# Optimization experiments

Hardware: AMD Instinct MI355X
Metric: run time of the kernel (lower is better)

The kernel has to match this reference:

```python
import jax, jax.numpy as jnp
import numpy as np

NUM_HEADS = 8


def setup_inputs() -> dict:
    key = jax.random.key(0)
    ks = jax.random.split(key, 5)
    B, C, H, W = 2, 256, 64, 64
    # 0.02 scaling keeps logits in a sane range so softmax is not one-hot
    return {
        "x": jax.random.normal(ks[0], (B, C, H, W), dtype=jnp.float32),
        "w_qkv": jax.random.normal(ks[1], (3 * C, C), dtype=jnp.float32) * 0.02,
        "b_qkv": jax.random.normal(ks[2], (3 * C,), dtype=jnp.float32) * 0.02,
        "w_proj": jax.random.normal(ks[3], (C, C), dtype=jnp.float32) * 0.02,
        "b_proj": jax.random.normal(ks[4], (C,), dtype=jnp.float32) * 0.02,
    }


def reference(x, w_qkv, b_qkv, w_proj, b_proj):
    B, C, H, W = x.shape
    N = H * W
    h = NUM_HEADS
    d = C // h
    # 1x1 conv == per-pixel linear: (B,C,H,W) -> (B,3C,H,W)
    qkv = jnp.einsum('oc,bchw->bohw', w_qkv, x) + b_qkv[None, :, None, None]
    qkv = qkv.reshape(B, 3, h, d, N)
    # q,k,v: (B, h, N, d)
    q = jnp.swapaxes(qkv[:, 0], -2, -1)
    k = jnp.swapaxes(qkv[:, 1], -2, -1)
    v = jnp.swapaxes(qkv[:, 2], -2, -1)
    scale = d ** (-0.5)
    attn = jax.nn.softmax(jnp.einsum('bhnd,bhmd->bhnm', q, k) * scale, axis=-1)
    out = jnp.einsum('bhnm,bhmd->bhnd', attn, v)  # (B, h, N, d)
    # faithful to torch: transpose(1,2) -> (B,N,h,d), then row-major reshape to (B,C,H,W)
    out = jnp.swapaxes(out, 1, 2).reshape(B, C, H, W)
    out = jnp.einsum('oc,bchw->bohw', w_proj, out) + b_proj[None, :, None, None]
    return out
```

## Files before the change

### kernel.cpp

```cpp
#include <hip/hip_runtime.h>
#include <hip/hip_bf16.h>


typedef __bf16 bf16;
typedef __bf16 bf16x4 __attribute__((ext_vector_type(4)));
typedef __bf16 bf16x8 __attribute__((ext_vector_type(8)));
typedef float  f32x4  __attribute__((ext_vector_type(4)));
typedef short  s16x4  __attribute__((ext_vector_type(4)));

#if __has_builtin(__builtin_amdgcn_mfma_f32_16x16x16bf16_1k)
#define HAVE_MFMA16 1
#endif

#if __has_builtin(__builtin_amdgcn_exp2f)
#define EXP2(x) __builtin_amdgcn_exp2f(x)
#else
#define EXP2(x) exp2f(x)
#endif

#define NS 4096
#define QSCALE (0.17677669529663687f * 1.4426950408889634f)

static __device__ inline unsigned pack2(float a, float b) {
  union { bf16 h[2]; unsigned u; } v;
  v.h[0] = (bf16)a; v.h[1] = (bf16)b;
  return v.u;
}

__global__ __launch_bounds__(256) void qkv_fused(
    const float* __restrict__ x, const float* __restrict__ w,
    const float* __restrict__ bias,
    bf16* __restrict__ qbuf, bf16* __restrict__ kbuf, bf16* __restrict__ vbuf)
{
  __shared__ bf16 As[64 * 264];
  __shared__ bf16 Bs[64 * 264];
  const int n0 = blockIdx.x * 64, o0 = blockIdx.y * 64, b = blockIdx.z;
  const int t = threadIdx.x;
  const int wv = t >> 6, L = t & 63, quad = L >> 4, lb = L & 15;

  {
    unsigned* A32 = (unsigned*)As;
    const int nj = (t & 15) * 4;
#pragma unroll
    for (int p = 0; p < 8; p++) {
      const int c = p * 32 + (t >> 4) * 2;
      const float* xr = x + ((size_t)(b * 256 + c)) * NS + n0 + nj;
      f32x4 va = *(const f32x4*)xr;
      f32x4 vb = *(const f32x4*)(xr + NS);
#pragma unroll
      for (int i = 0; i < 4; i++)
        A32[(nj + i) * 132 + (c >> 1)] = pack2(va[i], vb[i]);
    }
  }
  {
    const int cj = (t & 15) * 16;
#pragma unroll
    for (int p = 0; p < 4; p++) {
      const int r = p * 16 + (t >> 4);
      const float* wr = w + (size_t)(o0 + r) * 256 + cj;
      f32x4 w0 = *(const f32x4*)wr,       w1 = *(const f32x4*)(wr + 4);
      f32x4 w2 = *(const f32x4*)(wr + 8), w3 = *(const f32x4*)(wr + 12);
      bf16x8 lo, hi;
#pragma unroll
      for (int i = 0; i < 4; i++) {
        lo[i] = (bf16)w0[i]; lo[4 + i] = (bf16)w1[i];
        hi[i] = (bf16)w2[i]; hi[4 + i] = (bf16)w3[i];
      }
      *(bf16x8*)&Bs[r * 264 + cj] = lo;
      *(bf16x8*)&Bs[r * 264 + cj + 8] = hi;
    }
  }
  __syncthreads();

  f32x4 acc[4] = {};
#pragma unroll
  for (int ks = 0; ks < 8; ks++) {
    const bf16x8 bfr = *(const bf16x8*)&Bs[(wv * 16 + lb) * 264 + ks * 32 + quad * 8];
#pragma unroll
    for (int a = 0; a < 4; a++) {
      const bf16x8 afr = *(const bf16x8*)&As[(a * 16 + lb) * 264 + ks * 32 + quad * 8];
      acc[a] = __builtin_amdgcn_mfma_f32_16x16x32_bf16(afr, bfr, acc[a], 0, 0, 0);
    }
  }

  const int comp = o0 >> 8;
  const int o = o0 + wv * 16 + lb;
  const float bv = bias[o];
  if (comp < 2) {
    bf16* dst = (comp == 0) ? qbuf : kbuf;
    const float sc = (comp == 0) ? QSCALE : 1.0f;
    const int hh = (o & 255) >> 5, dd = o & 31;
    const size_t base = ((size_t)b * 8 + hh) * NS;
#pragma unroll
    for (int a = 0; a < 4; a++)
#pragma unroll
      for (int r = 0; r < 4; r++) {
        const int n = n0 + a * 16 + quad * 4 + r;
        dst[(base + n) * 32 + dd] = (bf16)((acc[a][r] + bv) * sc);
      }
  } else {
    __syncthreads();
    bf16* Vt2 = As;
#pragma unroll
    for (int a = 0; a < 4; a++)
#pragma unroll
      for (int r = 0; r < 4; r++)
        Vt2[(wv * 16 + lb) * 72 + a * 16 + quad * 4 + r] = (bf16)(acc[a][r] + bv);
    __syncthreads();
    const int row = t & 63;
    const int o2 = o0 + row;
    const int hh2 = (o2 & 255) >> 5, dd2 = o2 & 31;
    const int hc = (t >> 6) * 16;
    bf16x8 v0 = *(const bf16x8*)&Vt2[row * 72 + hc];
    bf16x8 v1 = *(const bf16x8*)&Vt2[row * 72 + hc + 8];
    bf16* vd = vbuf + (((size_t)b * 8 + hh2) * 32 + dd2) * NS + n0 + hc;
    *(bf16x8*)vd = v0;
    *(bf16x8*)(vd + 8) = v1;
  }
}

#define VT_OFF 2560
#define KV_SZ  (2560 + 32 * 72)

__global__ __launch_bounds__(256) void attn_kernel(
    const bf16* __restrict__ qbuf, const bf16* __restrict__ kbuf,
    const bf16* __restrict__ vbuf, float* __restrict__ pbuf,
    float* __restrict__ lbuf)
{
  __shared__ bf16 KV[2][KV_SZ];
#ifndef HAVE_MFMA16
  __shared__ bf16 Ps[4][16 * 72];
#endif

  const int qb = blockIdx.x;
  const int bh = blockIdx.y;
  const int half = blockIdx.z;
  const int kv0 = half * 2048;
  const bf16* Q  = qbuf + (size_t)bh * NS * 32;
  const bf16* K  = kbuf + (size_t)bh * NS * 32 + (size_t)kv0 * 32;
  const bf16* Vt = vbuf + (size_t)bh * 32 * NS + kv0;

  const int t = threadIdx.x;
  const int wv = t >> 6, L = t & 63, quad = L >> 4, lb = L & 15;
  const int qrow = qb * 128 + wv * 32;

  const bf16x8 qfrag0 = *(const bf16x8*)(Q + (size_t)(qrow + lb) * 32 + quad * 8);
  const bf16x8 qfrag1 = *(const bf16x8*)(Q + (size_t)(qrow + 16 + lb) * 32 + quad * 8);

  const int koff = (t >> 2) * 40 + (t & 3) * 8;
  const int voff = VT_OFF + (t >> 3) * 72 + (t & 7) * 8;
  const bf16* gk = K + (size_t)(t >> 2) * 32 + (t & 3) * 8;
  const bf16* gv = Vt + (size_t)(t >> 3) * NS + (t & 7) * 8;

  bf16x8 regk = *(const bf16x8*)gk;
  bf16x8 regv = *(const bf16x8*)gv;

  f32x4 oa0 = {0.f, 0.f, 0.f, 0.f}, oa1 = {0.f, 0.f, 0.f, 0.f};
  f32x4 oa2 = {0.f, 0.f, 0.f, 0.f}, oa3 = {0.f, 0.f, 0.f, 0.f};
  f32x4 oa4 = {0.f, 0.f, 0.f, 0.f}, oa5 = {0.f, 0.f, 0.f, 0.f};
  const f32x4 zero4 = {0.f, 0.f, 0.f, 0.f};
#ifdef HAVE_MFMA16
  const s16x4 ones = {(short)0x3F80, (short)0x3F80, (short)0x3F80, (short)0x3F80};
#else
  float l0_i = 0.f, l1_i = 0.f;
#endif

#pragma unroll 2
  for (int kt = 0; kt < 32; kt++) {
    const int buf = kt & 1;
    *(bf16x8*)&KV[buf][koff] = regk;
    *(bf16x8*)&KV[buf][voff] = regv;
    __syncthreads();
    if (kt < 31) {
      regk = *(const bf16x8*)(gk + (size_t)(kt + 1) * (64 * 32));
      regv = *(const bf16x8*)(gv + (size_t)(kt + 1) * 64);
    }

    f32x4 st0[4], st1[4];
#pragma unroll
    for (int bi = 0; bi < 4; bi++) {
      const bf16x8 kf = *(const bf16x8*)&KV[buf][(bi * 16 + lb) * 40 + quad * 8];
      st0[bi] = __builtin_amdgcn_mfma_f32_16x16x32_bf16(kf, qfrag0, zero4, 0, 0, 0);
      st1[bi] = __builtin_amdgcn_mfma_f32_16x16x32_bf16(kf, qfrag1, zero4, 0, 0, 0);
    }

#pragma unroll
    for (int bi = 0; bi < 4; bi++)
#pragma unroll
      for (int r = 0; r < 4; r++) {
        st0[bi][r] = EXP2(st0[bi][r]);
        st1[bi][r] = EXP2(st1[bi][r]);
      }

#ifdef HAVE_MFMA16
#pragma unroll
    for (int bi = 0; bi < 4; bi++) {
      bf16x4 pb0, pb1;
#pragma unroll
      for (int r = 0; r < 4; r++) {
        pb0[r] = (bf16)st0[bi][r];
        pb1[r] = (bf16)st1[bi][r];
      }
      const s16x4 pf0 = __builtin_bit_cast(s16x4, pb0);
      const s16x4 pf1 = __builtin_bit_cast(s16x4, pb1);
      const s16x4 vf0 = __builtin_bit_cast(s16x4,
          *(const bf16x4*)&KV[buf][VT_OFF + lb * 72 + bi * 16 + quad * 4]);
      const s16x4 vf1 = __builtin_bit_cast(s16x4,
          *(const bf16x4*)&KV[buf][VT_OFF + (16 + lb) * 72 + bi * 16 + quad * 4]);
      oa0 = __builtin_amdgcn_mfma_f32_16x16x16bf16_1k(pf0, vf0, oa0, 0, 0, 0);
      oa1 = __builtin_amdgcn_mfma_f32_16x16x16bf16_1k(pf0, vf1, oa1, 0, 0, 0);
      oa2 = __builtin_amdgcn_mfma_f32_16x16x16bf16_1k(pf0, ones, oa2, 0, 0, 0);
      oa3 = __builtin_amdgcn_mfma_f32_16x16x16bf16_1k(pf1, vf0, oa3, 0, 0, 0);
      oa4 = __builtin_amdgcn_mfma_f32_16x16x16bf16_1k(pf1, vf1, oa4, 0, 0, 0);
      oa5 = __builtin_amdgcn_mfma_f32_16x16x16bf16_1k(pf1, ones, oa5, 0, 0, 0);
    }
#else
    {
      float ls0 = 0.f, ls1 = 0.f;
#pragma unroll
      for (int bi = 0; bi < 4; bi++)
#pragma unroll
        for (int r = 0; r < 4; r++) { ls0 += st0[bi][r]; ls1 += st1[bi][r]; }
      l0_i += ls0; l1_i += ls1;
      bf16* P = &Ps[wv][0];
#pragma unroll
      for (int bi = 0; bi < 4; bi++) {
        bf16x4 pk;
#pragma unroll
        for (int r = 0; r < 4; r++) pk[r] = (bf16)st0[bi][r];
        *(bf16x4*)&P[lb * 72 + bi * 16 + quad * 4] = pk;
      }
#pragma unroll
      for (int ch = 0; ch < 2; ch++) {
        const bf16x8 pf  = *(const bf16x8*)&P[lb * 72 + ch * 32 + quad * 8];
        const bf16x8 vf0 = *(const bf16x8*)&KV[buf][VT_OFF + lb * 72 + ch * 32 + quad * 8];
        const bf16x8 vf1 = *(const bf16x8*)&KV[buf][VT_OFF + (16 + lb) * 72 + ch * 32 + quad * 8];
        oa0 = __builtin_amdgcn_mfma_f32_16x16x32_bf16(pf, vf0, oa0, 0, 0, 0);
        oa1 = __builtin_amdgcn_mfma_f32_16x16x32_bf16(pf, vf1, oa1, 0, 0, 0);
      }
#pragma unroll
      for (int bi = 0; bi < 4; bi++) {
        bf16x4 pk;
#pragma unroll
        for (int r = 0; r < 4; r++) pk[r] = (bf16)st1[bi][r];
        *(bf16x4*)&P[lb * 72 + bi * 16 + quad * 4] = pk;
      }
#pragma unroll
      for (int ch = 0; ch < 2; ch++) {
        const bf16x8 pf  = *(const bf16x8*)&P[lb * 72 + ch * 32 + quad * 8];
        const bf16x8 vf0 = *(const bf16x8*)&KV[buf][VT_OFF + lb * 72 + ch * 32 + quad * 8];
        const bf16x8 vf1 = *(const bf16x8*)&KV[buf][VT_OFF + (16 + lb) * 72 + ch * 32 + quad * 8];
        oa3 = __builtin_amdgcn_mfma_f32_16x16x32_bf16(pf, vf0, oa3, 0, 0, 0);
        oa4 = __builtin_amdgcn_mfma_f32_16x16x32_bf16(pf, vf1, oa4, 0, 0, 0);
      }
    }
#endif
  }

  const int b_ = bh >> 3;
  const int hh = bh & 7;
  float* pb = pbuf + ((size_t)(half * 2 + b_) * NS) * 256;
  float* lsum = lbuf + ((size_t)(half * 2 + b_) * NS) * 8;
#ifndef HAVE_MFMA16
  float lf0 = l0_i, lf1 = l1_i;
  lf0 += __shfl_xor(lf0, 16); lf0 += __shfl_xor(lf0, 32);
  lf1 += __shfl_xor(lf1, 16); lf1 += __shfl_xor(lf1, 32);
#endif
#pragma unroll
  for (int r = 0; r < 4; r++) {
    const int n0_ = qrow + quad * 4 + r;
    const int n1_ = n0_ + 16;
    float* d0 = pb + (size_t)n0_ * 256 + hh * 32;
    float* d1 = pb + (size_t)n1_ * 256 + hh * 32;
    d0[lb]      = oa0[r];
    d0[16 + lb] = oa1[r];
    d1[lb]      = oa3[r];
    d1[16 + lb] = oa4[r];
#ifdef HAVE_MFMA16
    if (lb == 0) {
      lsum[(size_t)n0_ * 8 + hh] = oa2[r];
      lsum[(size_t)n1_ * 8 + hh] = oa5[r];
    }
#else
    const float lr0 = __shfl(lf0, (quad << 4) | (quad * 4 + r));
    const float lr1 = __shfl(lf1, (quad << 4) | (quad * 4 + r));
    if (lb == 0) {
      lsum[(size_t)n0_ * 8 + hh] = lr0;
      lsum[(size_t)n1_ * 8 + hh] = lr1;
    }
#endif
  }
}

__global__ __launch_bounds__(256) void proj_fused(
    const float* __restrict__ pbuf, const float* __restrict__ lbuf,
    const float* __restrict__ w, const float* __restrict__ bias,
    float* __restrict__ out)
{
  __shared__ bf16 As[64 * 264];
  __shared__ bf16 Bs[64 * 264];
  const int ch0 = blockIdx.x * 64, o0 = blockIdx.y * 64;
  const int z = blockIdx.z, b = z >> 4, sHi = z & 15;
  const int t = threadIdx.x;
  const int wv = t >> 6, L = t & 63, quad = L >> 4, lb = L & 15;

  {
    const int cj = (t & 15) * 16;
#pragma unroll
    for (int p = 0; p < 4; p++) {
      const int r = p * 16 + (t >> 4);
      const float* wr = w + (size_t)(o0 + r) * 256 + cj;
      f32x4 w0 = *(const f32x4*)wr,       w1 = *(const f32x4*)(wr + 4);
      f32x4 w2 = *(const f32x4*)(wr + 8), w3 = *(const f32x4*)(wr + 12);
      bf16x8 lo, hi;
#pragma unroll
      for (int i = 0; i < 4; i++) {
        lo[i] = (bf16)w0[i]; lo[4 + i] = (bf16)w1[i];
        hi[i] = (bf16)w2[i]; hi[4 + i] = (bf16)w3[i];
      }
      *(bf16x8*)&As[r * 264 + cj] = lo;
      *(bf16x8*)&As[r * 264 + cj + 8] = hi;
    }
  }
  {
    const int chj = (t & 7) * 8;
    const int hh = (ch0 + chj) >> 5;
#pragma unroll
    for (int p = 0; p < 8; p++) {
      const int c = p * 32 + (t >> 3);
      const int n = c * 16 + sHi;
      const size_t row0 = (size_t)(0 * 2 + b) * NS + n;
      const size_t row1 = (size_t)(1 * 2 + b) * NS + n;
      const float* p0 = pbuf + row0 * 256 + ch0 + chj;
      const float* p1 = pbuf + row1 * 256 + ch0 + chj;
      f32x4 a0 = *(const f32x4*)p0,       a1 = *(const f32x4*)(p0 + 4);
      f32x4 c0 = *(const f32x4*)p1,       c1 = *(const f32x4*)(p1 + 4);
      const float l0 = lbuf[row0 * 8 + hh];
      const float l1 = lbuf[row1 * 8 + hh];
      const float inv = 1.0f / (l0 + l1);
#pragma unroll
      for (int i = 0; i < 4; i++) {
        Bs[(chj + i) * 264 + c]     = (bf16)((a0[i] + c0[i]) * inv);
        Bs[(chj + 4 + i) * 264 + c] = (bf16)((a1[i] + c1[i]) * inv);
      }
    }
  }
  __syncthreads();

  f32x4 acc[4] = {};
#pragma unroll
  for (int ks = 0; ks < 8; ks++) {
    const bf16x8 bfr = *(const bf16x8*)&Bs[(wv * 16 + lb) * 264 + ks * 32 + quad * 8];
#pragma unroll
    for (int a = 0; a < 4; a++) {
      const bf16x8 afr = *(const bf16x8*)&As[(a * 16 + lb) * 264 + ks * 32 + quad * 8];
      acc[a] = __builtin_amdgcn_mfma_f32_16x16x32_bf16(afr, bfr, acc[a], 0, 0, 0);
    }
  }

  const int ch = ch0 + wv * 16 + lb;
#pragma unroll
  for (int a = 0; a < 4; a++)
#pragma unroll
    for (int r = 0; r < 4; r++) {
      const int o = o0 + a * 16 + quad * 4 + r;
      out[((size_t)b * 256 + o) * NS + sHi * 256 + ch] = acc[a][r] + bias[o];
    }
}

extern "C" void kernel_launch(void* const* d_in, const int* in_sizes, int n_in,
                              void* d_out, int out_size, void* d_ws, size_t ws_size,
                              hipStream_t stream) {
  const float* x      = (const float*)d_in[0];
  const float* w_qkv  = (const float*)d_in[1];
  const float* b_qkv  = (const float*)d_in[2];
  const float* w_proj = (const float*)d_in[3];
  const float* b_proj = (const float*)d_in[4];
  float* out = (float*)d_out;

  char* ws = (char*)d_ws;
  const size_t MB = 1024 * 1024;
  bf16* qbuf  = (bf16*)(ws);
  bf16* kbuf  = (bf16*)(ws + 4 * MB);
  bf16* vbuf  = (bf16*)(ws + 8 * MB);
  float* pbuf = (float*)(ws + 12 * MB);
  float* lbuf = (float*)(ws + 28 * MB);

  qkv_fused<<<dim3(64, 12, 2), 256, 0, stream>>>(x, w_qkv, b_qkv, qbuf, kbuf, vbuf);
  attn_kernel<<<dim3(32, 16, 2), 256, 0, stream>>>(qbuf, kbuf, vbuf, pbuf, lbuf);
  proj_fused<<<dim3(4, 4, 32), 256, 0, stream>>>(pbuf, lbuf, w_proj, b_proj, out);
}
```

Before: 150.8 us.

## Split attention KV range into four parts and raise MFMA wave priority

The attention kernel now splits the 4096-key range into four 1024-key chunks instead of two, doubling the grid to 2048 blocks. Each chunk writes partial outputs and row sums, and the projection kernel reduces four partials instead of two. It also sets launch bounds to 8 waves-per-EU occupancy and raises wave priority around the compute section. This should improve occupancy and load balance on the many-CU device, at the cost of doubled partial-buffer traffic (fp32, 16 MB more) and extra reduction reads in the projection stage.

```diff
diff --git a/kernel.cpp b/kernel.cpp
--- a/kernel.cpp
+++ b/kernel.cpp
@@ -122,7 +122,7 @@
 #define VT_OFF 2560
 #define KV_SZ  (2560 + 32 * 72)
 
-__global__ __launch_bounds__(256) void attn_kernel(
+__global__ __launch_bounds__(256, 8) void attn_kernel(
     const bf16* __restrict__ qbuf, const bf16* __restrict__ kbuf,
     const bf16* __restrict__ vbuf, float* __restrict__ pbuf,
     float* __restrict__ lbuf)
@@ -134,8 +134,8 @@
 
   const int qb = blockIdx.x;
   const int bh = blockIdx.y;
-  const int half = blockIdx.z;
-  const int kv0 = half * 2048;
+  const int part = blockIdx.z;
+  const int kv0 = part * 1024;
   const bf16* Q  = qbuf + (size_t)bh * NS * 32;
   const bf16* K  = kbuf + (size_t)bh * NS * 32 + (size_t)kv0 * 32;
   const bf16* Vt = vbuf + (size_t)bh * 32 * NS + kv0;
@@ -166,16 +166,17 @@
 #endif
 
 #pragma unroll 2
-  for (int kt = 0; kt < 32; kt++) {
+  for (int kt = 0; kt < 16; kt++) {
     const int buf = kt & 1;
     *(bf16x8*)&KV[buf][koff] = regk;
     *(bf16x8*)&KV[buf][voff] = regv;
     __syncthreads();
-    if (kt < 31) {
+    if (kt < 15) {
       regk = *(const bf16x8*)(gk + (size_t)(kt + 1) * (64 * 32));
       regv = *(const bf16x8*)(gv + (size_t)(kt + 1) * 64);
     }
 
+    __builtin_amdgcn_s_setprio(1);
     f32x4 st0[4], st1[4];
 #pragma unroll
     for (int bi = 0; bi < 4; bi++) {
@@ -255,12 +256,13 @@
       }
     }
 #endif
+    __builtin_amdgcn_s_setprio(0);
   }
 
   const int b_ = bh >> 3;
   const int hh = bh & 7;
-  float* pb = pbuf + ((size_t)(half * 2 + b_) * NS) * 256;
-  float* lsum = lbuf + ((size_t)(half * 2 + b_) * NS) * 8;
+  float* pb = pbuf + ((size_t)(part * 2 + b_) * NS) * 256;
+  float* lsum = lbuf + ((size_t)(part * 2 + b_) * NS) * 8;
 #ifndef HAVE_MFMA16
   float lf0 = l0_i, lf1 = l1_i;
   lf0 += __shfl_xor(lf0, 16); lf0 += __shfl_xor(lf0, 32);
@@ -329,19 +331,21 @@
     for (int p = 0; p < 8; p++) {
       const int c = p * 32 + (t >> 3);
       const int n = c * 16 + sHi;
-      const size_t row0 = (size_t)(0 * 2 + b) * NS + n;
-      const size_t row1 = (size_t)(1 * 2 + b) * NS + n;
-      const float* p0 = pbuf + row0 * 256 + ch0 + chj;
-      const float* p1 = pbuf + row1 * 256 + ch0 + chj;
-      f32x4 a0 = *(const f32x4*)p0,       a1 = *(const f32x4*)(p0 + 4);
-      f32x4 c0 = *(const f32x4*)p1,       c1 = *(const f32x4*)(p1 + 4);
-      const float l0 = lbuf[row0 * 8 + hh];
-      const float l1 = lbuf[row1 * 8 + hh];
-      const float inv = 1.0f / (l0 + l1);
+      f32x4 s0 = {0.f, 0.f, 0.f, 0.f}, s1 = {0.f, 0.f, 0.f, 0.f};
+      float lt = 0.f;
+#pragma unroll
+      for (int hq = 0; hq < 4; hq++) {
+        const size_t row = (size_t)(hq * 2 + b) * NS + n;
+        const float* pp = pbuf + row * 256 + ch0 + chj;
+        s0 += *(const f32x4*)pp;
+        s1 += *(const f32x4*)(pp + 4);
+        lt += lbuf[row * 8 + hh];
+      }
+      const float inv = 1.0f / lt;
 #pragma unroll
       for (int i = 0; i < 4; i++) {
-        Bs[(chj + i) * 264 + c]     = (bf16)((a0[i] + c0[i]) * inv);
-        Bs[(chj + 4 + i) * 264 + c] = (bf16)((a1[i] + c1[i]) * inv);
+        Bs[(chj + i) * 264 + c]     = (bf16)(s0[i] * inv);
+        Bs[(chj + 4 + i) * 264 + c] = (bf16)(s1[i] * inv);
       }
     }
   }
@@ -384,9 +388,9 @@
   bf16* kbuf  = (bf16*)(ws + 4 * MB);
   bf16* vbuf  = (bf16*)(ws + 8 * MB);
   float* pbuf = (float*)(ws + 12 * MB);
-  float* lbuf = (float*)(ws + 28 * MB);
+  float* lbuf = (float*)(ws + 44 * MB);
 
   qkv_fused<<<dim3(64, 12, 2), 256, 0, stream>>>(x, w_qkv, b_qkv, qbuf, kbuf, vbuf);
-  attn_kernel<<<dim3(32, 16, 2), 256, 0, stream>>>(qbuf, kbuf, vbuf, pbuf, lbuf);
+  attn_kernel<<<dim3(32, 16, 4), 256, 0, stream>>>(qbuf, kbuf, vbuf, pbuf, lbuf);
   proj_fused<<<dim3(4, 4, 32), 256, 0, stream>>>(pbuf, lbuf, w_proj, b_proj, out);
 }
```

New measurement: 241.6 us. +60.2%, slower.
